# Kernel tuning notes

Measured on AMD Instinct MI355X. Metric: run time of the kernel, lower is better.

Reference implementation:

```python
import jax, jax.numpy as jnp
import numpy as np

B, T, IDIM, HDIM = 16, 512, 80, 512
TEMPER = 10.0


def _windows(key_pad, n_shifts, win):
    idx = jnp.arange(n_shifts)[:, None] + jnp.arange(win)[None, :]
    return key_pad[..., idx]


def setup_inputs() -> dict:
    key = jax.random.key(0)
    k1, k2, k3 = jax.random.split(key, 3)
    x = jax.random.normal(k1, (B, T, IDIM), dtype=jnp.float32)
    y = jax.random.normal(k2, (B, T, IDIM), dtype=jnp.float32)
    # xavier-uniform fc1 weight, zero bias (per initialize())
    limit = float(np.sqrt(6.0 / (IDIM + HDIM)))
    fc1_w = jax.random.uniform(k3, (HDIM, IDIM), jnp.float32, -limit, limit)
    fc1_b = jnp.zeros((HDIM,), jnp.float32)
    return {"x": x, "y": y, "fc1_w": fc1_w, "fc1_b": fc1_b}


def reference(x, y, fc1_w, fc1_b):
    idim = x.shape[-1]
    pad = idim - 1                 # idim_q - 1
    S = 2 * idim - 1               # idim_k + idim_q - 1 shift positions

    # ---- _pad_for_shift: (B,T,S,idim) sliding windows over padded key ----
    key_pad = jnp.pad(x, ((0, 0), (0, 0), (pad, pad)))
    kpt = _windows(key_pad, S, idim)                        # (B,T,S,idim)

    # ---- _simiality: cosine similarity per shift, max over shifts ----
    q = y[..., None, :]                                     # (B,T,1,idim)
    denom = jnp.linalg.norm(q, axis=-1) * jnp.linalg.norm(kpt, axis=-1)
    sim = jnp.sum(q * kpt, axis=-1) / denom                 # (B,T,S)
    sim = jnp.where(jnp.isnan(sim), 0.0, sim)
    sim_max = jnp.max(sim, axis=-1)                         # (B,T)
    sim_max_idx = jnp.argmax(sim, axis=-1)                  # (B,T)

    # ---- select best-shift window (argaug, scale=False, single theta) ----
    x_aug = jnp.take_along_axis(kpt, sim_max_idx[..., None, None], axis=-2)[..., 0, :]  # (B,T,idim)

    # ---- temp_softmax attention (detached in original) ----
    score = x_aug * y
    attn = jax.nn.softmax(score / TEMPER, axis=-1)
    attn = jnp.where(jnp.isnan(attn), 0.0, attn)
    attn = jax.lax.stop_gradient(attn)
    x_attn = x_aug * attn                                   # (B,T,idim)

    # ---- _reverse_pad_for_shift: undo the shift on x_attn ----
    kp2 = jnp.pad(x_attn, ((0, 0), (0, 0), (pad, pad)))
    kpt2 = _windows(kp2, S, idim)                           # (B,T,S,idim)
    rev_idx = 2 * idim - 2 - sim_max_idx                    # p_aug = shift index
    x_ele = jnp.take_along_axis(kpt2, rev_idx[..., None, None], axis=-2)[..., 0, :]

    # ---- fc1 MLP on shifted-attended features ----
    h = jnp.einsum('bti,hi->bth', x_attn, fc1_w) + fc1_b    # (B,T,hdim)
    return h
```

## Files before the change

### kernel.cpp

```cpp
#include <hip/hip_runtime.h>
#include <math.h>

#define BT    8192
#define IDIM  80
#define HDIM  512
#define SPAN  159
#define PADX  320
#define KPAD  96
#define LDK   104

typedef unsigned short ushort_t;
typedef __attribute__((ext_vector_type(8))) short short8;
typedef __attribute__((ext_vector_type(4))) float floatx4;
typedef __attribute__((ext_vector_type(4))) unsigned short ushort4v;

__device__ inline ushort_t f2bf(float f) {
    union { float f; unsigned int i; } v; v.f = f;
    unsigned int x = v.i;
    return (ushort_t)((x + 0x7fffu + ((x >> 16) & 1u)) >> 16);
}

__global__ __launch_bounds__(256) void k_attn(const float* __restrict__ x,
                                              const float* __restrict__ y,
                                              float* __restrict__ xattn) {
    __shared__ float xp[4][PADX];
    __shared__ float ysm[4][IDIM];
    const int w    = threadIdx.x >> 6;
    const int lane = threadIdx.x & 63;
    const int row  = blockIdx.x * 4 + w;
    const float* xr = x + (size_t)row * IDIM;
    const float* yr = y + (size_t)row * IDIM;

    for (int j = lane; j < PADX; j += 64) xp[w][j] = 0.f;
    __syncthreads();
    float yy = 0.f;
    if (lane < 20) {
        float4 xv = *(const float4*)(xr + lane * 4);
        float4 yv = *(const float4*)(yr + lane * 4);
        int b = 79 + lane * 4;
        xp[w][b + 0] = xv.x; xp[w][b + 1] = xv.y;
        xp[w][b + 2] = xv.z; xp[w][b + 3] = xv.w;
        int c = lane * 4;
        ysm[w][c + 0] = yv.x; ysm[w][c + 1] = yv.y;
        ysm[w][c + 2] = yv.z; ysm[w][c + 3] = yv.w;
        yy = yv.x * yv.x + yv.y * yv.y + yv.z * yv.z + yv.w * yv.w;
    }
    __syncthreads();
    #pragma unroll
    for (int off = 32; off; off >>= 1) yy += __shfl_xor(yy, off);

    const float* xpw = xp[w];
    const float* ysw = ysm[w];
    float d0 = 0.f, d1 = 0.f, d2 = 0.f, n0 = 0.f, n1 = 0.f, n2 = 0.f;
    #pragma unroll 4
    for (int i = 0; i < IDIM; ++i) {
        float yv = ysw[i];
        float a0 = xpw[lane + i];
        float a1 = xpw[lane + 64 + i];
        float a2 = xpw[lane + 128 + i];
        d0 += yv * a0; n0 += a0 * a0;
        d1 += yv * a1; n1 += a1 * a1;
        d2 += yv * a2; n2 += a2 * a2;
    }
    float s0 = (n0 > 0.f) ? d0 / sqrtf(yy * n0) : 0.f;
    float s1 = (n1 > 0.f) ? d1 / sqrtf(yy * n1) : 0.f;
    float s2 = (lane < 31) ? ((n2 > 0.f) ? d2 / sqrtf(yy * n2) : 0.f) : -INFINITY;

    float bv = s0; int bi = lane;
    if (s1 > bv) { bv = s1; bi = lane + 64; }
    if (s2 > bv) { bv = s2; bi = lane + 128; }
    #pragma unroll
    for (int off = 32; off; off >>= 1) {
        float ov = __shfl_xor(bv, off);
        int   oi = __shfl_xor(bi, off);
        if (ov > bv || (ov == bv && oi < bi)) { bv = ov; bi = oi; }
    }

    float xa0 = xpw[bi + lane];
    float yv0 = ysw[lane];
    float z0  = (xa0 * yv0) / 10.0f;
    float xa1 = 0.f, z1 = -INFINITY;
    if (lane < 16) {
        xa1 = xpw[bi + lane + 64];
        float yv1 = ysw[lane + 64];
        z1 = (xa1 * yv1) / 10.0f;
    }
    float m = fmaxf(z0, z1);
    #pragma unroll
    for (int off = 32; off; off >>= 1) m = fmaxf(m, __shfl_xor(m, off));
    float e0 = expf(z0 - m);
    float e1 = (lane < 16) ? expf(z1 - m) : 0.f;
    float es = e0 + e1;
    #pragma unroll
    for (int off = 32; off; off >>= 1) es += __shfl_xor(es, off);
    float inv = 1.0f / es;

    float* orow = xattn + (size_t)row * IDIM;
    orow[lane] = xa0 * (e0 * inv);
    if (lane < 16) orow[lane + 64] = xa1 * (e1 * inv);
}

__global__ __launch_bounds__(256) void k_gemm_mfma(const float* __restrict__ xattn,
                                                   const float* __restrict__ wmat,
                                                   const float* __restrict__ bias,
                                                   float* __restrict__ out) {
    __shared__ __align__(16) ushort_t Abf[64][LDK];
    __shared__ __align__(16) ushort_t Wbf[64][LDK];
    const int tid = threadIdx.x;
    const int rb  = blockIdx.x * 64;
    const int cb  = blockIdx.y * 64;

    if (tid < 64) {
        ushort4v z = {0, 0, 0, 0};
        *(ushort4v*)&Abf[tid][80] = z; *(ushort4v*)&Abf[tid][84] = z;
        *(ushort4v*)&Abf[tid][88] = z; *(ushort4v*)&Abf[tid][92] = z;
        *(ushort4v*)&Wbf[tid][80] = z; *(ushort4v*)&Wbf[tid][84] = z;
        *(ushort4v*)&Wbf[tid][88] = z; *(ushort4v*)&Wbf[tid][92] = z;
    }
    #pragma unroll
    for (int q = 0; q < 5; ++q) {
        int idx = q * 256 + tid;
        int r   = idx / 20;
        int kp  = (idx % 20) * 4;
        float4 av = *(const float4*)(xattn + (size_t)(rb + r) * IDIM + kp);
        ushort4v ab = { f2bf(av.x), f2bf(av.y), f2bf(av.z), f2bf(av.w) };
        *(ushort4v*)&Abf[r][kp] = ab;
        float4 wv = *(const float4*)(wmat + (size_t)(cb + r) * IDIM + kp);
        ushort4v wb = { f2bf(wv.x), f2bf(wv.y), f2bf(wv.z), f2bf(wv.w) };
        *(ushort4v*)&Wbf[r][kp] = wb;
    }
    __syncthreads();

    const int wv   = tid >> 6;
    const int lane = tid & 63;
    const int m    = lane & 15;
    const int q4   = lane >> 4;

    short8 af[3];
    #pragma unroll
    for (int kt = 0; kt < 3; ++kt)
        af[kt] = *(const short8*)&Abf[16 * wv + m][q4 * 8 + kt * 32];

    floatx4 acc[4] = {{0.f,0.f,0.f,0.f}, {0.f,0.f,0.f,0.f},
                      {0.f,0.f,0.f,0.f}, {0.f,0.f,0.f,0.f}};
    #pragma unroll
    for (int ct = 0; ct < 4; ++ct) {
        #pragma unroll
        for (int kt = 0; kt < 3; ++kt) {
            short8 bf = *(const short8*)&Wbf[ct * 16 + m][q4 * 8 + kt * 32];
            acc[ct] = __builtin_amdgcn_mfma_f32_16x16x32_bf16(af[kt], bf, acc[ct], 0, 0, 0);
        }
    }

    #pragma unroll
    for (int ct = 0; ct < 4; ++ct) {
        int col = cb + ct * 16 + m;
        float bsv = bias[col];
        int row0 = rb + 16 * wv + q4 * 4;
        #pragma unroll
        for (int i = 0; i < 4; ++i)
            out[(size_t)(row0 + i) * HDIM + col] = acc[ct][i] + bsv;
    }
}

extern "C" void kernel_launch(void* const* d_in, const int* in_sizes, int n_in,
                              void* d_out, int out_size, void* d_ws, size_t ws_size,
                              hipStream_t stream) {
    const float* x  = (const float*)d_in[0];
    const float* y  = (const float*)d_in[1];
    const float* wm = (const float*)d_in[2];
    const float* bs = (const float*)d_in[3];
    float* out   = (float*)d_out;
    float* xattn = (float*)d_ws;

    k_attn<<<dim3(BT / 4), 256, 0, stream>>>(x, y, xattn);
    k_gemm_mfma<<<dim3(BT / 64, HDIM / 64), 256, 0, stream>>>(xattn, wm, bs, out);
}
```

Baseline: 83.30 us.

## Use prefix sums for window norms and store bf16 intermediate activations

The attention kernel now gets each shifted window's squared norm from a wave-level prefix scan over the padded row, replacing a per-window accumulation loop. The dot-product loop is reworked to read y as float4. The intermediate x_attn is written as bf16, so the GEMM loads half the bytes and skips its own conversion. Prefix-sum differences can lose floating-point precision, which could perturb the argmax selection.

```diff
diff --git a/kernel.cpp b/kernel.cpp
--- a/kernel.cpp
+++ b/kernel.cpp
@@ -6,7 +6,6 @@
 #define HDIM  512
 #define SPAN  159
 #define PADX  320
-#define KPAD  96
 #define LDK   104
 
 typedef unsigned short ushort_t;
@@ -22,9 +21,10 @@
 
 __global__ __launch_bounds__(256) void k_attn(const float* __restrict__ x,
                                               const float* __restrict__ y,
-                                              float* __restrict__ xattn) {
+                                              ushort_t* __restrict__ xattn) {
     __shared__ float xp[4][PADX];
     __shared__ float ysm[4][IDIM];
+    __shared__ float Pex[4][PADX];
     const int w    = threadIdx.x >> 6;
     const int lane = threadIdx.x & 63;
     const int row  = blockIdx.x * 4 + w;
@@ -51,17 +51,41 @@
 
     const float* xpw = xp[w];
     const float* ysw = ysm[w];
-    float d0 = 0.f, d1 = 0.f, d2 = 0.f, n0 = 0.f, n1 = 0.f, n2 = 0.f;
-    #pragma unroll 4
-    for (int i = 0; i < IDIM; ++i) {
-        float yv = ysw[i];
-        float a0 = xpw[lane + i];
-        float a1 = xpw[lane + 64 + i];
-        float a2 = xpw[lane + 128 + i];
-        d0 += yv * a0; n0 += a0 * a0;
-        d1 += yv * a1; n1 += a1 * a1;
-        d2 += yv * a2; n2 += a2 * a2;
-    }
+
+    {
+        float carry = 0.f;
+        #pragma unroll
+        for (int k = 0; k < 5; ++k) {
+            float v  = xpw[lane + 64 * k];
+            float sq = v * v;
+            float incl = sq;
+            #pragma unroll
+            for (int off = 1; off < 64; off <<= 1) {
+                float t = __shfl_up(incl, off);
+                if (lane >= off) incl += t;
+            }
+            Pex[w][64 * k + lane] = carry + incl - sq;
+            carry += __shfl(incl, 63);
+        }
+    }
+    __syncthreads();
+
+    float d0 = 0.f, d1 = 0.f, d2 = 0.f;
+    #pragma unroll
+    for (int i = 0; i < IDIM; i += 4) {
+        float4 yv = *(const float4*)&ysw[i];
+        d0 += yv.x * xpw[lane + i]     + yv.y * xpw[lane + i + 1]
+            + yv.z * xpw[lane + i + 2] + yv.w * xpw[lane + i + 3];
+        d1 += yv.x * xpw[lane + 64 + i]     + yv.y * xpw[lane + 64 + i + 1]
+            + yv.z * xpw[lane + 64 + i + 2] + yv.w * xpw[lane + 64 + i + 3];
+        d2 += yv.x * xpw[lane + 128 + i]     + yv.y * xpw[lane + 128 + i + 1]
+            + yv.z * xpw[lane + 128 + i + 2] + yv.w * xpw[lane + 128 + i + 3];
+    }
+    const float* Pw = Pex[w];
+    float n0 = Pw[lane + 80]  - Pw[lane];
+    float n1 = Pw[lane + 144] - Pw[lane + 64];
+    float n2 = Pw[lane + 208] - Pw[lane + 128];
+
     float s0 = (n0 > 0.f) ? d0 / sqrtf(yy * n0) : 0.f;
     float s1 = (n1 > 0.f) ? d1 / sqrtf(yy * n1) : 0.f;
     float s2 = (lane < 31) ? ((n2 > 0.f) ? d2 / sqrtf(yy * n2) : 0.f) : -INFINITY;
@@ -95,12 +119,12 @@
     for (int off = 32; off; off >>= 1) es += __shfl_xor(es, off);
     float inv = 1.0f / es;
 
-    float* orow = xattn + (size_t)row * IDIM;
-    orow[lane] = xa0 * (e0 * inv);
-    if (lane < 16) orow[lane + 64] = xa1 * (e1 * inv);
-}
-
-__global__ __launch_bounds__(256) void k_gemm_mfma(const float* __restrict__ xattn,
+    ushort_t* orow = xattn + (size_t)row * IDIM;
+    orow[lane] = f2bf(xa0 * (e0 * inv));
+    if (lane < 16) orow[lane + 64] = f2bf(xa1 * (e1 * inv));
+}
+
+__global__ __launch_bounds__(256) void k_gemm_mfma(const ushort_t* __restrict__ xattn,
                                                    const float* __restrict__ wmat,
                                                    const float* __restrict__ bias,
                                                    float* __restrict__ out) {
@@ -118,13 +142,20 @@
         *(ushort4v*)&Wbf[tid][88] = z; *(ushort4v*)&Wbf[tid][92] = z;
     }
     #pragma unroll
+    for (int q = 0; q < 3; ++q) {
+        int idx = q * 256 + tid;
+        if (idx < 640) {
+            int r  = idx / 10;
+            int kp = (idx % 10) * 8;
+            uint4 v = *(const uint4*)(xattn + (size_t)(rb + r) * IDIM + kp);
+            *(uint4*)&Abf[r][kp] = v;
+        }
+    }
+    #pragma unroll
     for (int q = 0; q < 5; ++q) {
         int idx = q * 256 + tid;
         int r   = idx / 20;
         int kp  = (idx % 20) * 4;
-        float4 av = *(const float4*)(xattn + (size_t)(rb + r) * IDIM + kp);
-        ushort4v ab = { f2bf(av.x), f2bf(av.y), f2bf(av.z), f2bf(av.w) };
-        *(ushort4v*)&Abf[r][kp] = ab;
         float4 wv = *(const float4*)(wmat + (size_t)(cb + r) * IDIM + kp);
         ushort4v wb = { f2bf(wv.x), f2bf(wv.y), f2bf(wv.z), f2bf(wv.w) };
         *(ushort4v*)&Wbf[r][kp] = wb;
@@ -170,8 +201,8 @@
     const float* y  = (const float*)d_in[1];
     const float* wm = (const float*)d_in[2];
     const float* bs = (const float*)d_in[3];
-    float* out   = (float*)d_out;
-    float* xattn = (float*)d_ws;
+    float* out = (float*)d_out;
+    ushort_t* xattn = (ushort_t*)d_ws;
 
     k_attn<<<dim3(BT / 4), 256, 0, stream>>>(x, y, xattn);
     k_gemm_mfma<<<dim3(BT / 64, HDIM / 64), 256, 0, stream>>>(xattn, wm, bs, out);
```

New measurement: 90.68 us. +8.9%, slower.
